# Performance work log

Measured on AMD Instinct MI355X. Metric: run time of the kernel, lower is better.

## Reference

```python
import jax, jax.numpy as jnp
import numpy as np
from jax import lax

X, H, L, VT, ET = 4096, 1024, 8, 512, 1024


def setup_inputs() -> dict:
    key = jax.random.key(0)
    ks = jax.random.split(key, 10)
    stdv = 1.0 / np.sqrt(H)
    u = lambda k, shape, s: jax.random.uniform(k, shape, jnp.float32, -s, s)
    inp = {
        "input_x": jax.random.normal(ks[0], (X,), jnp.float32),
        "h_prev": jax.random.normal(ks[1], (L, H), jnp.float32),
        # fused gate weights: order [input, forget, output, state] along the 4H axis
        "Wg": u(ks[2], (L, 4 * H, X + 2 * H), stdv),
        # combined bias = Linear bias + extra b_* parameter (same math, one tensor)
        "bg": u(ks[3], (L, 4 * H), 2.0 * stdv),
        "old_state": u(ks[4], (L, H), stdv),
        "Wy": u(ks[5], (VT, L * H), 1.0 / np.sqrt(L * H)),
        "by": u(ks[6], (VT,), 1.0 / np.sqrt(L * H)),
        "We": u(ks[7], (ET, L * H), 1.0 / np.sqrt(L * H)),
        "be": u(ks[8], (ET,), 1.0 / np.sqrt(L * H)),
    }
    return inp


def reference(input_x, h_prev, Wg, bg, old_state, Wy, by, We, be):
    def step(prev_layer, per_layer):
        W, b, c_old, h_t = per_layer
        # semicolon_input = [input_x ; previous_time ; previous_layer]
        z = jnp.concatenate([input_x, h_t, prev_layer])  # (X+2H,)
        gates = W @ z + b                                 # (4H,) fused 4 GEMVs
        i_g, f_g, o_g, s_g = jnp.split(gates, 4)
        new_state = jax.nn.sigmoid(f_g) * c_old + jax.nn.sigmoid(i_g) * jnp.tanh(s_g)
        new_hidden = jax.nn.sigmoid(o_g) * jnp.tanh(new_state)
        return new_hidden, new_hidden

    init = jnp.zeros((H,), input_x.dtype)  # hidden_previous_layer starts at 0
    _, hidden = lax.scan(step, init, (Wg, bg, old_state, h_prev))  # (L, H)
    flat = hidden.reshape(L * H)
    output = Wy @ flat + by
    interface = We @ flat + be
    return output, interface
```

## Files before the change

kernel.cpp:

```cpp
#include <hip/hip_runtime.h>
#include <hip/hip_bf16.h>
#include <cstddef>


#define XDIM 4096
#define HDIM 1024
#define LNUM 8
#define ZDIM 6144
#define ZPAR 5120
#define VT 512
#define ET 1024

__device__ __forceinline__ float sigmoidf_(float v) {
    return 1.0f / (1.0f + expf(-v));
}

__global__ __launch_bounds__(256) void partial_gates_kernel(
    const float* __restrict__ x,
    const float* __restrict__ hprev,
    const float* __restrict__ Wg,
    const float* __restrict__ bg,
    float* __restrict__ partial)
{
    __shared__ float z[ZPAR];

    const int block_row0 = blockIdx.x * 4;
    const int l = block_row0 >> 12;

    for (int i = threadIdx.x; i < XDIM / 4; i += blockDim.x)
        reinterpret_cast<float4*>(z)[i] = reinterpret_cast<const float4*>(x)[i];
    for (int i = threadIdx.x; i < HDIM / 4; i += blockDim.x)
        reinterpret_cast<float4*>(z + XDIM)[i] =
            reinterpret_cast<const float4*>(hprev + l * HDIM)[i];
    __syncthreads();

    const int wave = threadIdx.x >> 6;
    const int lane = threadIdx.x & 63;
    const int row  = block_row0 + wave;

    const float4* __restrict__ Wrow =
        reinterpret_cast<const float4*>(Wg + (size_t)row * ZDIM);
    const float4* __restrict__ z4 = reinterpret_cast<const float4*>(z);

    float acc = 0.0f;
    #pragma unroll 4
    for (int p = 0; p < 20; ++p) {
        float4 w  = Wrow[p * 64 + lane];
        float4 zv = z4[p * 64 + lane];
        acc += w.x * zv.x + w.y * zv.y + w.z * zv.z + w.w * zv.w;
    }
    #pragma unroll
    for (int off = 32; off > 0; off >>= 1)
        acc += __shfl_down(acc, off, 64);

    if (lane == 0)
        partial[row] = acc + bg[row];
}

__global__ __launch_bounds__(256) void layer_step_kernel(
    const float* __restrict__ Wg,
    const float* __restrict__ partial,
    const float* __restrict__ old_state,
    const float* __restrict__ hidden_prev,
    float* __restrict__ hidden_out,
    int l, int has_prev)
{
    __shared__ float hp[HDIM];

    if (has_prev) {
        reinterpret_cast<float4*>(hp)[threadIdx.x] =
            reinterpret_cast<const float4*>(hidden_prev)[threadIdx.x];
    }
    __syncthreads();

    const int wave = threadIdx.x >> 6;
    const int lane = threadIdx.x & 63;
    const int h    = blockIdx.x * 4 + wave;

    const float4* __restrict__ hp4 = reinterpret_cast<const float4*>(hp);

    float g[4];
    #pragma unroll
    for (int q = 0; q < 4; ++q) {
        float acc = 0.0f;
        if (has_prev) {
            const size_t row = (size_t)l * 4096 + (size_t)q * HDIM + h;
            const float4* __restrict__ Wrow =
                reinterpret_cast<const float4*>(Wg + row * ZDIM + ZPAR);
            #pragma unroll
            for (int p = 0; p < 4; ++p) {
                float4 w  = Wrow[p * 64 + lane];
                float4 zv = hp4[p * 64 + lane];
                acc += w.x * zv.x + w.y * zv.y + w.z * zv.z + w.w * zv.w;
            }
        }
        #pragma unroll
        for (int off = 32; off > 0; off >>= 1)
            acc += __shfl_down(acc, off, 64);
        g[q] = acc + partial[(size_t)l * 4096 + (size_t)q * HDIM + h];
    }

    if (lane == 0) {
        const float ig = sigmoidf_(g[0]);
        const float fg = sigmoidf_(g[1]);
        const float og = sigmoidf_(g[2]);
        const float sg = tanhf(g[3]);
        const float ns = fg * old_state[l * HDIM + h] + ig * sg;
        hidden_out[h] = og * tanhf(ns);
    }
}

__global__ __launch_bounds__(256) void head_kernel(
    const float* __restrict__ Wy, const float* __restrict__ by,
    const float* __restrict__ We, const float* __restrict__ be,
    const float* __restrict__ flat,
    float* __restrict__ out)
{
    __shared__ float z[LNUM * HDIM];

    for (int i = threadIdx.x; i < (LNUM * HDIM) / 4; i += blockDim.x)
        reinterpret_cast<float4*>(z)[i] = reinterpret_cast<const float4*>(flat)[i];
    __syncthreads();

    const int wave = threadIdx.x >> 6;
    const int lane = threadIdx.x & 63;
    const int row  = blockIdx.x * 4 + wave;

    const float* __restrict__ W;
    float b;
    if (row < VT) { W = Wy + (size_t)row * (LNUM * HDIM);          b = by[row]; }
    else          { W = We + (size_t)(row - VT) * (LNUM * HDIM);   b = be[row - VT]; }

    const float4* __restrict__ W4 = reinterpret_cast<const float4*>(W);
    const float4* __restrict__ z4 = reinterpret_cast<const float4*>(z);

    float acc = 0.0f;
    #pragma unroll 4
    for (int p = 0; p < 32; ++p) {
        float4 w  = W4[p * 64 + lane];
        float4 zv = z4[p * 64 + lane];
        acc += w.x * zv.x + w.y * zv.y + w.z * zv.z + w.w * zv.w;
    }
    #pragma unroll
    for (int off = 32; off > 0; off >>= 1)
        acc += __shfl_down(acc, off, 64);

    if (lane == 0)
        out[row] = acc + b;
}

extern "C" void kernel_launch(void* const* d_in, const int* in_sizes, int n_in,
                              void* d_out, int out_size, void* d_ws, size_t ws_size,
                              hipStream_t stream)
{
    const float* x         = (const float*)d_in[0];
    const float* hprev     = (const float*)d_in[1];
    const float* Wg        = (const float*)d_in[2];
    const float* bg        = (const float*)d_in[3];
    const float* old_state = (const float*)d_in[4];
    const float* Wy        = (const float*)d_in[5];
    const float* by        = (const float*)d_in[6];
    const float* We        = (const float*)d_in[7];
    const float* be        = (const float*)d_in[8];
    float* out = (float*)d_out;

    float* partial = (float*)d_ws;
    float* hidden  = partial + LNUM * 4096;

    partial_gates_kernel<<<8192, 256, 0, stream>>>(x, hprev, Wg, bg, partial);

    for (int l = 0; l < LNUM; ++l) {
        layer_step_kernel<<<256, 256, 0, stream>>>(
            Wg, partial, old_state,
            (l > 0) ? (hidden + (size_t)(l - 1) * HDIM) : hidden ,
            hidden + (size_t)l * HDIM, l, (l > 0) ? 1 : 0);
    }

    head_kernel<<<(VT + ET) / 4, 256, 0, stream>>>(Wy, by, We, be, hidden, out);
}
```

Measured before the change: 191.7 us.

## Fuse gate precompute and layer scan into one persistent kernel with atomic flags

Replaces the partial-gates kernel and eight per-layer launches with a single kernel of 1024 blocks, one per hidden unit. Each block computes its four gate rows for every layer and waits on a global atomic counter for the previous layer's hidden vector before adding the recurrent term. This removes launch overhead and the round trip through the partial buffer, and lets the input-part GEMV of later layers overlap the wait. It relies on all 1024 blocks being co-resident to avoid deadlock, and each layer's GEMV now runs on the critical path rather than being precomputed in bulk.

```diff
diff --git a/kernel.cpp b/kernel.cpp
--- a/kernel.cpp
+++ b/kernel.cpp
@@ -15,98 +15,90 @@
     return 1.0f / (1.0f + expf(-v));
 }
 
-__global__ __launch_bounds__(256) void partial_gates_kernel(
+__global__ void zero_cnt_kernel(int* __restrict__ cnt) {
+    if (threadIdx.x < LNUM) cnt[threadIdx.x] = 0;
+}
+
+__global__ __launch_bounds__(256, 4) void fused_scan_kernel(
     const float* __restrict__ x,
     const float* __restrict__ hprev,
     const float* __restrict__ Wg,
     const float* __restrict__ bg,
-    float* __restrict__ partial)
+    const float* __restrict__ old_state,
+    float* __restrict__ hidden,
+    int* __restrict__ cnt)
 {
     __shared__ float z[ZPAR];
+    __shared__ float hp[HDIM];
+    __shared__ float gred[4];
 
-    const int block_row0 = blockIdx.x * 4;
-    const int l = block_row0 >> 12;
+    const int tid  = threadIdx.x;
+    const int wave = tid >> 6;
+    const int lane = tid & 63;
+    const int h    = blockIdx.x;
 
-    for (int i = threadIdx.x; i < XDIM / 4; i += blockDim.x)
+    for (int i = tid; i < XDIM / 4; i += 256)
         reinterpret_cast<float4*>(z)[i] = reinterpret_cast<const float4*>(x)[i];
-    for (int i = threadIdx.x; i < HDIM / 4; i += blockDim.x)
-        reinterpret_cast<float4*>(z + XDIM)[i] =
-            reinterpret_cast<const float4*>(hprev + l * HDIM)[i];
-    __syncthreads();
 
-    const int wave = threadIdx.x >> 6;
-    const int lane = threadIdx.x & 63;
-    const int row  = block_row0 + wave;
+    for (int l = 0; l < LNUM; ++l) {
+        __syncthreads();
 
-    const float4* __restrict__ Wrow =
-        reinterpret_cast<const float4*>(Wg + (size_t)row * ZDIM);
-    const float4* __restrict__ z4 = reinterpret_cast<const float4*>(z);
+        reinterpret_cast<float4*>(z + XDIM)[tid] =
+            reinterpret_cast<const float4*>(hprev + (size_t)l * HDIM)[tid];
+        __syncthreads();
 
-    float acc = 0.0f;
-    #pragma unroll 4
-    for (int p = 0; p < 20; ++p) {
-        float4 w  = Wrow[p * 64 + lane];
-        float4 zv = z4[p * 64 + lane];
-        acc += w.x * zv.x + w.y * zv.y + w.z * zv.z + w.w * zv.w;
-    }
-    #pragma unroll
-    for (int off = 32; off > 0; off >>= 1)
-        acc += __shfl_down(acc, off, 64);
+        const size_t row = (size_t)l * 4096 + (size_t)wave * HDIM + h;
+        const float4* __restrict__ W4 =
+            reinterpret_cast<const float4*>(Wg + row * ZDIM);
+        const float4* __restrict__ z4 = reinterpret_cast<const float4*>(z);
 
-    if (lane == 0)
-        partial[row] = acc + bg[row];
-}
+        float acc = 0.0f;
+        #pragma unroll 4
+        for (int p = 0; p < 20; ++p) {
+            float4 w = W4[p * 64 + lane];
+            float4 v = z4[p * 64 + lane];
+            acc += w.x * v.x + w.y * v.y + w.z * v.z + w.w * v.w;
+        }
 
-__global__ __launch_bounds__(256) void layer_step_kernel(
-    const float* __restrict__ Wg,
-    const float* __restrict__ partial,
-    const float* __restrict__ old_state,
-    const float* __restrict__ hidden_prev,
-    float* __restrict__ hidden_out,
-    int l, int has_prev)
-{
-    __shared__ float hp[HDIM];
+        if (l > 0) {
+            if (tid == 0) {
+                while (__hip_atomic_load(&cnt[l - 1], __ATOMIC_ACQUIRE,
+                                         __HIP_MEMORY_SCOPE_AGENT) < HDIM)
+                    __builtin_amdgcn_s_sleep(1);
+            }
+            __syncthreads();
+            reinterpret_cast<float4*>(hp)[tid] =
+                reinterpret_cast<const float4*>(hidden + (size_t)(l - 1) * HDIM)[tid];
+            __syncthreads();
 
-    if (has_prev) {
-        reinterpret_cast<float4*>(hp)[threadIdx.x] =
-            reinterpret_cast<const float4*>(hidden_prev)[threadIdx.x];
-    }
-    __syncthreads();
-
-    const int wave = threadIdx.x >> 6;
-    const int lane = threadIdx.x & 63;
-    const int h    = blockIdx.x * 4 + wave;
-
-    const float4* __restrict__ hp4 = reinterpret_cast<const float4*>(hp);
-
-    float g[4];
-    #pragma unroll
-    for (int q = 0; q < 4; ++q) {
-        float acc = 0.0f;
-        if (has_prev) {
-            const size_t row = (size_t)l * 4096 + (size_t)q * HDIM + h;
-            const float4* __restrict__ Wrow =
+            const float4* __restrict__ C4 =
                 reinterpret_cast<const float4*>(Wg + row * ZDIM + ZPAR);
+            const float4* __restrict__ h4 = reinterpret_cast<const float4*>(hp);
             #pragma unroll
             for (int p = 0; p < 4; ++p) {
-                float4 w  = Wrow[p * 64 + lane];
-                float4 zv = hp4[p * 64 + lane];
-                acc += w.x * zv.x + w.y * zv.y + w.z * zv.z + w.w * zv.w;
+                float4 w = C4[p * 64 + lane];
+                float4 v = h4[p * 64 + lane];
+                acc += w.x * v.x + w.y * v.y + w.z * v.z + w.w * v.w;
             }
         }
+
         #pragma unroll
         for (int off = 32; off > 0; off >>= 1)
             acc += __shfl_down(acc, off, 64);
-        g[q] = acc + partial[(size_t)l * 4096 + (size_t)q * HDIM + h];
-    }
+        if (lane == 0)
+            gred[wave] = acc + bg[row];
+        __syncthreads();
 
-    if (lane == 0) {
-        const float ig = sigmoidf_(g[0]);
-        const float fg = sigmoidf_(g[1]);
-        const float og = sigmoidf_(g[2]);
-        const float sg = tanhf(g[3]);
-        const float ns = fg * old_state[l * HDIM + h] + ig * sg;
-        hidden_out[h] = og * tanhf(ns);
+        if (tid == 0) {
+            const float ig = sigmoidf_(gred[0]);
+            const float fg = sigmoidf_(gred[1]);
+            const float og = sigmoidf_(gred[2]);
+            const float sg = tanhf(gred[3]);
+            const float ns = fg * old_state[(size_t)l * HDIM + h] + ig * sg;
+            hidden[(size_t)l * HDIM + h] = og * tanhf(ns);
+            __threadfence();
+            atomicAdd(&cnt[l], 1);
+        }
     }
 }
 
@@ -128,8 +120,8 @@
 
     const float* __restrict__ W;
     float b;
-    if (row < VT) { W = Wy + (size_t)row * (LNUM * HDIM);          b = by[row]; }
-    else          { W = We + (size_t)(row - VT) * (LNUM * HDIM);   b = be[row - VT]; }
+    if (row < VT) { W = Wy + (size_t)row * (LNUM * HDIM);        b = by[row]; }
+    else          { W = We + (size_t)(row - VT) * (LNUM * HDIM); b = be[row - VT]; }
 
     const float4* __restrict__ W4 = reinterpret_cast<const float4*>(W);
     const float4* __restrict__ z4 = reinterpret_cast<const float4*>(z);
@@ -137,9 +129,9 @@
     float acc = 0.0f;
     #pragma unroll 4
     for (int p = 0; p < 32; ++p) {
-        float4 w  = W4[p * 64 + lane];
-        float4 zv = z4[p * 64 + lane];
-        acc += w.x * zv.x + w.y * zv.y + w.z * zv.z + w.w * zv.w;
+        float4 w = W4[p * 64 + lane];
+        float4 v = z4[p * 64 + lane];
+        acc += w.x * v.x + w.y * v.y + w.z * v.z + w.w * v.w;
     }
     #pragma unroll
     for (int off = 32; off > 0; off >>= 1)
@@ -164,17 +156,13 @@
     const float* be        = (const float*)d_in[8];
     float* out = (float*)d_out;
 
-    float* partial = (float*)d_ws;
-    float* hidden  = partial + LNUM * 4096;
+    float* hidden = (float*)d_ws;
+    int*   cnt    = (int*)d_ws + LNUM * HDIM;
 
-    partial_gates_kernel<<<8192, 256, 0, stream>>>(x, hprev, Wg, bg, partial);
+    zero_cnt_kernel<<<1, 64, 0, stream>>>(cnt);
 
-    for (int l = 0; l < LNUM; ++l) {
-        layer_step_kernel<<<256, 256, 0, stream>>>(
-            Wg, partial, old_state,
-            (l > 0) ? (hidden + (size_t)(l - 1) * HDIM) : hidden ,
-            hidden + (size_t)l * HDIM, l, (l > 0) ? 1 : 0);
-    }
+    fused_scan_kernel<<<1024, 256, 0, stream>>>(
+        x, hprev, Wg, bg, old_state, hidden, cnt);
 
     head_kernel<<<(VT + ET) / 4, 256, 0, stream>>>(Wy, by, We, be, hidden, out);
 }
```

Measured after the change: 516.7 us. +169.6%, slower.
